# Performance work log

Hardware: AMD Instinct MI355X
Metric: run time of the kernel (lower is better)

## Reference

```python
import jax, jax.numpy as jnp
import numpy as np

N_NODES = 50000
N_EDGES = 800000
F_IN = 128
HID = 128
N_GRAPHS = 256


def setup_inputs() -> dict:
    key = jax.random.key(0)
    ks = jax.random.split(key, 12)
    gx = jax.random.normal(ks[0], (N_NODES, F_IN), dtype=jnp.float32)
    edge_index = jax.random.randint(ks[1], (2, N_EDGES), 0, N_NODES, dtype=jnp.int64)
    batch = jnp.sort(jax.random.randint(ks[2], (N_NODES,), 0, N_GRAPHS, dtype=jnp.int64))
    edge_attr = jax.random.uniform(ks[3], (N_EDGES,), dtype=jnp.float32)
    s1 = 1.0 / np.sqrt(F_IN)
    s2 = 1.0 / np.sqrt(HID)
    W1 = jax.random.uniform(ks[4], (F_IN, HID), jnp.float32, -s1, s1)
    b1 = jnp.zeros((HID,), jnp.float32)
    W2 = jax.random.uniform(ks[5], (HID, HID), jnp.float32, -s2, s2)
    b2 = jnp.zeros((HID,), jnp.float32)
    W3 = jax.random.uniform(ks[6], (HID, HID), jnp.float32, -s2, s2)
    b3 = jnp.zeros((HID,), jnp.float32)
    return {"gx": gx, "edge_index": edge_index, "batch": batch, "edge_attr": edge_attr,
            "W1": W1, "b1": b1, "W2": W2, "b2": b2, "W3": W3, "b3": b3}


def _gcn_conv(x, W, b, row, col, edge_weight, n_nodes):
    # PyG GCNConv with add_self_loops=False:
    #   deg[i] = sum of edge_weight over edges with dst == i
    #   norm_e = deg^{-1/2}[row] * w_e * deg^{-1/2}[col]
    #   out[i] = sum_{e: col_e == i} norm_e * (x @ W)[row_e] + b
    deg = jax.ops.segment_sum(edge_weight, col, num_segments=n_nodes)
    dinv = jnp.where(deg > 0, jax.lax.rsqrt(deg), 0.0)
    norm = dinv[row] * edge_weight * dinv[col]  # [E]
    h = x @ W  # [N, H]
    msg = h[row] * norm[:, None]  # [E, H] gather + scale
    out = jax.ops.segment_sum(msg, col, num_segments=n_nodes)  # scatter-add
    return out + b


def reference(gx, edge_index, batch, edge_attr, W1, b1, W2, b2, W3, b3):
    row, col = edge_index[0], edge_index[1]
    n = gx.shape[0]
    # dropout layers are in eval mode (identity) for a deterministic reference
    h = jax.nn.relu(_gcn_conv(gx, W1, b1, row, col, edge_attr, n))
    h = jax.nn.relu(_gcn_conv(h, W2, b2, row, col, edge_attr, n))
    h = _gcn_conv(h, W3, b3, row, col, edge_attr, n)
    readout = jax.ops.segment_sum(h, batch, num_segments=N_GRAPHS)  # global_add_pool
    return h, readout
```

## Files before the change

kernel.cpp:

```cpp
#include <hip/hip_runtime.h>

#define FEAT 128

typedef __attribute__((ext_vector_type(8))) short short8;
typedef __attribute__((ext_vector_type(4))) float f32x4;

__device__ __forceinline__ unsigned int bf16rtn(float f) {
    unsigned int u = __float_as_uint(f);
    return (u + 0x7fffu + ((u >> 16) & 1u)) >> 16;
}
__device__ __forceinline__ float bf16tof(unsigned int h) { return __uint_as_float(h << 16); }
__device__ __forceinline__ float bf16lo(unsigned int v) { return __uint_as_float(v << 16); }
__device__ __forceinline__ float bf16hi(unsigned int v) { return __uint_as_float(v & 0xffff0000u); }

__global__ __launch_bounds__(256) void hist_kernel(const int* __restrict__ col,
                                                   int* __restrict__ ghist,
                                                   int E, int nblk, int nbuck) {
    __shared__ int h[256];
    const int t = threadIdx.x, b = blockIdx.x;
    h[t] = 0;
    __syncthreads();
    const int base = b * 4096;
#pragma unroll
    for (int i = 0; i < 16; ++i) {
        int e = base + i * 256 + t;
        if (e < E) atomicAdd(&h[col[e] >> 8], 1);
    }
    __syncthreads();
    if (t < nbuck) ghist[t * nblk + b] = h[t];
}

__global__ __launch_bounds__(256) void scan_block_kernel(const int* __restrict__ cnt,
                                                         int* __restrict__ out,
                                                         int* __restrict__ bsum, int M) {
    __shared__ int s[256];
    int t = threadIdx.x;
    int i = blockIdx.x * 256 + t;
    int own = (i < M) ? cnt[i] : 0;
    s[t] = own;
    for (int off = 1; off < 256; off <<= 1) {
        __syncthreads();
        int v = (t >= off) ? s[t - off] : 0;
        __syncthreads();
        s[t] += v;
    }
    __syncthreads();
    if (i < M) out[i] = s[t] - own;
    if (t == 255) bsum[blockIdx.x] = s[255];
}

__global__ __launch_bounds__(256) void scan_bsum_kernel(int* __restrict__ bsum, int nb) {
    __shared__ int s[256];
    int t = threadIdx.x;
    int own = (t < nb) ? bsum[t] : 0;
    s[t] = own;
    for (int off = 1; off < 256; off <<= 1) {
        __syncthreads();
        int v = (t >= off) ? s[t - off] : 0;
        __syncthreads();
        s[t] += v;
    }
    __syncthreads();
    if (t < nb) bsum[t] = s[t] - own;
}

__global__ __launch_bounds__(256) void scatter1_kernel(const int* __restrict__ row,
                                                       const int* __restrict__ col,
                                                       const float* __restrict__ ew,
                                                       const int* __restrict__ gsc,
                                                       const int* __restrict__ bsum,
                                                       uint2* __restrict__ bedge,
                                                       int E, int nblk, int nbuck) {
    __shared__ int cur[256];
    const int t = threadIdx.x, b = blockIdx.x;
    if (t < nbuck) {
        int idx = t * nblk + b;
        cur[t] = gsc[idx] + bsum[idx >> 8];
    }
    __syncthreads();
    const int base = b * 4096;
#pragma unroll
    for (int i = 0; i < 16; ++i) {
        int e = base + i * 256 + t;
        if (e < E) {
            int c = col[e];
            int slot = atomicAdd(&cur[c >> 8], 1);
            bedge[slot] = make_uint2(((unsigned)c << 16) | (unsigned)row[e],
                                     __float_as_uint(ew[e]));
        }
    }
}

__global__ __launch_bounds__(256) void bucket_kernel(const uint2* __restrict__ bedge,
                                                     const int* __restrict__ gsc,
                                                     const int* __restrict__ bsum,
                                                     int* __restrict__ rowptr,
                                                     float* __restrict__ dinv,
                                                     uint2* __restrict__ sedge,
                                                     int N, int E, int nblk, int nbuck) {
    __shared__ int lcnt[256];
    __shared__ float lw[256];
    __shared__ int lscan[256];
    __shared__ int lcur[256];
    __shared__ float ldv[256];

    const int d = blockIdx.x, t = threadIdx.x;
    const int i0 = d * nblk;
    const int base = gsc[i0] + bsum[i0 >> 8];
    int end;
    if (d == nbuck - 1) end = E;
    else {
        const int i1 = (d + 1) * nblk;
        end = gsc[i1] + bsum[i1 >> 8];
    }

    lcnt[t] = 0;
    lw[t] = 0.f;
    __syncthreads();
    for (int i = base + t; i < end; i += 256) {
        uint2 p = bedge[i];
        int c = (p.x >> 16) & 255;
        atomicAdd(&lcnt[c], 1);
        atomicAdd(&lw[c], __uint_as_float(p.y));
    }
    __syncthreads();
    int own = lcnt[t];
    lscan[t] = own;
    for (int off = 1; off < 256; off <<= 1) {
        __syncthreads();
        int v = (t >= off) ? lscan[t - off] : 0;
        __syncthreads();
        lscan[t] += v;
    }
    __syncthreads();
    int excl = lscan[t] - own;
    lcur[t] = base + excl;
    float wsum = lw[t];
    float dv = (wsum > 0.f) ? rsqrtf(wsum) : 0.f;
    ldv[t] = dv;
    int node = d * 256 + t;
    if (node < N) {
        rowptr[node] = base + excl;
        dinv[node] = dv;
    }
    if (d == nbuck - 1 && t == 0) rowptr[N] = E;
    __syncthreads();
    for (int i = base + t; i < end; i += 256) {
        uint2 p = bedge[i];
        int c = (p.x >> 16) & 255;
        int slot = atomicAdd(&lcur[c], 1);
        sedge[slot] = make_uint2(p.x & 0xFFFFu,
                                 __float_as_uint(__uint_as_float(p.y) * ldv[c]));
    }
}

__global__ void convw_kernel(const float* __restrict__ W0, const float* __restrict__ W1,
                             const float* __restrict__ W2,
                             unsigned short* __restrict__ Whi, unsigned short* __restrict__ Wlo) {
    int i = blockIdx.x * blockDim.x + threadIdx.x;
    int which = blockIdx.y;
    const float* W = (which == 0) ? W0 : (which == 1) ? W1 : W2;
    int c = i >> 7, k = i & 127;
    float w = W[(size_t)k * FEAT + c];
    unsigned int h = bf16rtn(w);
    size_t off = (size_t)which * 16384 + (size_t)c * FEAT + k;
    Whi[off] = (unsigned short)h;
    Wlo[off] = (unsigned short)bf16rtn(w - bf16tof(h));
}

__global__ __launch_bounds__(256) void gemm_mfma_kernel(
    const float* __restrict__ X,
    const unsigned short* __restrict__ Wthi, const unsigned short* __restrict__ Wtlo,
    const float* __restrict__ dinv,
    unsigned int* __restrict__ hb,
    int N)
{
    __shared__ unsigned short wh[64 * 128];
    __shared__ unsigned short wl[64 * 128];

    const int tid = threadIdx.x;
    const int r0 = blockIdx.x * 64;
    const int cb = blockIdx.y;

#pragma unroll
    for (int it = 0; it < 4; ++it) {
        int idx = it * 256 + tid;
        int c = idx >> 4;
        int k8 = (idx & 15) * 8;
        int sw = k8 ^ ((c & 7) << 3);
        size_t src = (size_t)(cb * 64 + c) * FEAT + k8;
        *(short8*)&wh[c * 128 + sw] = *(const short8*)(Wthi + src);
        *(short8*)&wl[c * 128 + sw] = *(const short8*)(Wtlo + src);
    }
    __syncthreads();

    const int lane = tid & 63;
    const int wv = tid >> 6;
    const int m = lane & 15;
    const int quad = lane >> 4;
    const int arow = wv * 16 + m;
    const int grow = r0 + arow;
    const float* xrow = X + (size_t)grow * FEAT;

    f32x4 acc[4];
#pragma unroll
    for (int ct = 0; ct < 4; ++ct) acc[ct] = (f32x4){0.f, 0.f, 0.f, 0.f};

#pragma unroll
    for (int kt = 0; kt < 4; ++kt) {
        const int k0 = kt * 32 + quad * 8;
        float4 va = make_float4(0.f, 0.f, 0.f, 0.f);
        float4 vb = make_float4(0.f, 0.f, 0.f, 0.f);
        if (grow < N) {
            va = *(const float4*)(xrow + k0);
            vb = *(const float4*)(xrow + k0 + 4);
        }
        unsigned int h0 = bf16rtn(va.x), h1 = bf16rtn(va.y);
        unsigned int h2 = bf16rtn(va.z), h3 = bf16rtn(va.w);
        unsigned int h4 = bf16rtn(vb.x), h5 = bf16rtn(vb.y);
        unsigned int h6 = bf16rtn(vb.z), h7 = bf16rtn(vb.w);
        short8 ah, al;
        ah[0] = (short)h0; ah[1] = (short)h1; ah[2] = (short)h2; ah[3] = (short)h3;
        ah[4] = (short)h4; ah[5] = (short)h5; ah[6] = (short)h6; ah[7] = (short)h7;
        al[0] = (short)bf16rtn(va.x - bf16tof(h0));
        al[1] = (short)bf16rtn(va.y - bf16tof(h1));
        al[2] = (short)bf16rtn(va.z - bf16tof(h2));
        al[3] = (short)bf16rtn(va.w - bf16tof(h3));
        al[4] = (short)bf16rtn(vb.x - bf16tof(h4));
        al[5] = (short)bf16rtn(vb.y - bf16tof(h5));
        al[6] = (short)bf16rtn(vb.z - bf16tof(h6));
        al[7] = (short)bf16rtn(vb.w - bf16tof(h7));
#pragma unroll
        for (int ct = 0; ct < 4; ++ct) {
            int bc = ct * 16 + m;
            int bw = k0 ^ ((bc & 7) << 3);
            short8 bh = *(const short8*)&wh[bc * 128 + bw];
            short8 bl = *(const short8*)&wl[bc * 128 + bw];
            acc[ct] = __builtin_amdgcn_mfma_f32_16x16x32_bf16(ah, bh, acc[ct], 0, 0, 0);
            acc[ct] = __builtin_amdgcn_mfma_f32_16x16x32_bf16(ah, bl, acc[ct], 0, 0, 0);
            acc[ct] = __builtin_amdgcn_mfma_f32_16x16x32_bf16(al, bh, acc[ct], 0, 0, 0);
        }
    }

    const int rbase = wv * 16 + quad * 4;
    const int grb = r0 + rbase;
    float dv0, dv1, dv2, dv3;
    if (grb + 3 < N) {
        float4 d4 = *(const float4*)(dinv + grb);
        dv0 = d4.x; dv1 = d4.y; dv2 = d4.z; dv3 = d4.w;
    } else {
        dv0 = (grb + 0 < N) ? dinv[grb + 0] : 0.f;
        dv1 = (grb + 1 < N) ? dinv[grb + 1] : 0.f;
        dv2 = (grb + 2 < N) ? dinv[grb + 2] : 0.f;
        dv3 = (grb + 3 < N) ? dinv[grb + 3] : 0.f;
    }

    __syncthreads();
    unsigned short* cl = wh;
#pragma unroll
    for (int ct = 0; ct < 4; ++ct) {
        cl[(rbase + 0) * 72 + ct * 16 + m] = (unsigned short)bf16rtn(acc[ct][0] * dv0);
        cl[(rbase + 1) * 72 + ct * 16 + m] = (unsigned short)bf16rtn(acc[ct][1] * dv1);
        cl[(rbase + 2) * 72 + ct * 16 + m] = (unsigned short)bf16rtn(acc[ct][2] * dv2);
        cl[(rbase + 3) * 72 + ct * 16 + m] = (unsigned short)bf16rtn(acc[ct][3] * dv3);
    }
    __syncthreads();
#pragma unroll
    for (int it = 0; it < 2; ++it) {
        int idx = it * 256 + tid;
        int r = idx >> 3;
        int c4 = (idx & 7) * 4;
        int gr = r0 + r;
        if (gr < N) {
            uint4 pv = *(const uint4*)&cl[r * 72 + c4 * 2];
            *(uint4*)(hb + (size_t)gr * 64 + cb * 32 + c4) = pv;
        }
    }
}

template <int RELU>
__global__ __launch_bounds__(256) void agg_kernel(
    const int* __restrict__ rowptr, const uint2* __restrict__ sedge,
    const uint4* __restrict__ hb4,
    const float* __restrict__ bias,
    float* __restrict__ outX, int N)
{
    const int node = blockIdx.x * 16 + (threadIdx.x >> 4);
    if (node >= N) return;
    const int j = threadIdx.x & 15;
    const int s = rowptr[node];
    const int e = rowptr[node + 1];

    float a0 = 0.f, a1 = 0.f, a2 = 0.f, a3 = 0.f;
    float a4 = 0.f, a5 = 0.f, a6 = 0.f, a7 = 0.f;

    for (int gb = s; gb < e; gb += 8) {
        uint2 m0, m1, m2, m3, m4, m5, m6, m7;
        if (gb + 8 <= e) {
            m0 = sedge[gb + 0]; m1 = sedge[gb + 1];
            m2 = sedge[gb + 2]; m3 = sedge[gb + 3];
            m4 = sedge[gb + 4]; m5 = sedge[gb + 5];
            m6 = sedge[gb + 6]; m7 = sedge[gb + 7];
        } else {
            const uint2 z = make_uint2(0u, 0u);
            m0 = (gb + 0 < e) ? sedge[gb + 0] : z;
            m1 = (gb + 1 < e) ? sedge[gb + 1] : z;
            m2 = (gb + 2 < e) ? sedge[gb + 2] : z;
            m3 = (gb + 3 < e) ? sedge[gb + 3] : z;
            m4 = (gb + 4 < e) ? sedge[gb + 4] : z;
            m5 = (gb + 5 < e) ? sedge[gb + 5] : z;
            m6 = (gb + 6 < e) ? sedge[gb + 6] : z;
            m7 = (gb + 7 < e) ? sedge[gb + 7] : z;
        }
        uint4 v0 = hb4[(size_t)m0.x * 16 + j];
        uint4 v1 = hb4[(size_t)m1.x * 16 + j];
        uint4 v2 = hb4[(size_t)m2.x * 16 + j];
        uint4 v3 = hb4[(size_t)m3.x * 16 + j];
        uint4 v4 = hb4[(size_t)m4.x * 16 + j];
        uint4 v5 = hb4[(size_t)m5.x * 16 + j];
        uint4 v6 = hb4[(size_t)m6.x * 16 + j];
        uint4 v7 = hb4[(size_t)m7.x * 16 + j];
        float w0 = __uint_as_float(m0.y), w1 = __uint_as_float(m1.y);
        float w2 = __uint_as_float(m2.y), w3 = __uint_as_float(m3.y);
        float w4 = __uint_as_float(m4.y), w5 = __uint_as_float(m5.y);
        float w6 = __uint_as_float(m6.y), w7 = __uint_as_float(m7.y);
        a0 = fmaf(w0, bf16lo(v0.x), a0); a1 = fmaf(w0, bf16hi(v0.x), a1);
        a2 = fmaf(w0, bf16lo(v0.y), a2); a3 = fmaf(w0, bf16hi(v0.y), a3);
        a4 = fmaf(w0, bf16lo(v0.z), a4); a5 = fmaf(w0, bf16hi(v0.z), a5);
        a6 = fmaf(w0, bf16lo(v0.w), a6); a7 = fmaf(w0, bf16hi(v0.w), a7);
        a0 = fmaf(w1, bf16lo(v1.x), a0); a1 = fmaf(w1, bf16hi(v1.x), a1);
        a2 = fmaf(w1, bf16lo(v1.y), a2); a3 = fmaf(w1, bf16hi(v1.y), a3);
        a4 = fmaf(w1, bf16lo(v1.z), a4); a5 = fmaf(w1, bf16hi(v1.z), a5);
        a6 = fmaf(w1, bf16lo(v1.w), a6); a7 = fmaf(w1, bf16hi(v1.w), a7);
        a0 = fmaf(w2, bf16lo(v2.x), a0); a1 = fmaf(w2, bf16hi(v2.x), a1);
        a2 = fmaf(w2, bf16lo(v2.y), a2); a3 = fmaf(w2, bf16hi(v2.y), a3);
        a4 = fmaf(w2, bf16lo(v2.z), a4); a5 = fmaf(w2, bf16hi(v2.z), a5);
        a6 = fmaf(w2, bf16lo(v2.w), a6); a7 = fmaf(w2, bf16hi(v2.w), a7);
        a0 = fmaf(w3, bf16lo(v3.x), a0); a1 = fmaf(w3, bf16hi(v3.x), a1);
        a2 = fmaf(w3, bf16lo(v3.y), a2); a3 = fmaf(w3, bf16hi(v3.y), a3);
        a4 = fmaf(w3, bf16lo(v3.z), a4); a5 = fmaf(w3, bf16hi(v3.z), a5);
        a6 = fmaf(w3, bf16lo(v3.w), a6); a7 = fmaf(w3, bf16hi(v3.w), a7);
        a0 = fmaf(w4, bf16lo(v4.x), a0); a1 = fmaf(w4, bf16hi(v4.x), a1);
        a2 = fmaf(w4, bf16lo(v4.y), a2); a3 = fmaf(w4, bf16hi(v4.y), a3);
        a4 = fmaf(w4, bf16lo(v4.z), a4); a5 = fmaf(w4, bf16hi(v4.z), a5);
        a6 = fmaf(w4, bf16lo(v4.w), a6); a7 = fmaf(w4, bf16hi(v4.w), a7);
        a0 = fmaf(w5, bf16lo(v5.x), a0); a1 = fmaf(w5, bf16hi(v5.x), a1);
        a2 = fmaf(w5, bf16lo(v5.y), a2); a3 = fmaf(w5, bf16hi(v5.y), a3);
        a4 = fmaf(w5, bf16lo(v5.z), a4); a5 = fmaf(w5, bf16hi(v5.z), a5);
        a6 = fmaf(w5, bf16lo(v5.w), a6); a7 = fmaf(w5, bf16hi(v5.w), a7);
        a0 = fmaf(w6, bf16lo(v6.x), a0); a1 = fmaf(w6, bf16hi(v6.x), a1);
        a2 = fmaf(w6, bf16lo(v6.y), a2); a3 = fmaf(w6, bf16hi(v6.y), a3);
        a4 = fmaf(w6, bf16lo(v6.z), a4); a5 = fmaf(w6, bf16hi(v6.z), a5);
        a6 = fmaf(w6, bf16lo(v6.w), a6); a7 = fmaf(w6, bf16hi(v6.w), a7);
        a0 = fmaf(w7, bf16lo(v7.x), a0); a1 = fmaf(w7, bf16hi(v7.x), a1);
        a2 = fmaf(w7, bf16lo(v7.y), a2); a3 = fmaf(w7, bf16hi(v7.y), a3);
        a4 = fmaf(w7, bf16lo(v7.z), a4); a5 = fmaf(w7, bf16hi(v7.z), a5);
        a6 = fmaf(w7, bf16lo(v7.w), a6); a7 = fmaf(w7, bf16hi(v7.w), a7);
    }

    float4 bv0 = ((const float4*)bias)[j * 2];
    float4 bv1 = ((const float4*)bias)[j * 2 + 1];
    a0 += bv0.x; a1 += bv0.y; a2 += bv0.z; a3 += bv0.w;
    a4 += bv1.x; a5 += bv1.y; a6 += bv1.z; a7 += bv1.w;
    if (RELU) {
        a0 = fmaxf(a0, 0.f); a1 = fmaxf(a1, 0.f);
        a2 = fmaxf(a2, 0.f); a3 = fmaxf(a3, 0.f);
        a4 = fmaxf(a4, 0.f); a5 = fmaxf(a5, 0.f);
        a6 = fmaxf(a6, 0.f); a7 = fmaxf(a7, 0.f);
    }
    *(float4*)(outX + (size_t)node * FEAT + j * 8)     = make_float4(a0, a1, a2, a3);
    *(float4*)(outX + (size_t)node * FEAT + j * 8 + 4) = make_float4(a4, a5, a6, a7);
}

__global__ __launch_bounds__(256) void readout_kernel(const float* __restrict__ h,
                                                      const int* __restrict__ batch,
                                                      float* __restrict__ ro, int N) {
    __shared__ float part[128];
    const int g = blockIdx.x;
    const int j = threadIdx.x & 127;
    const int half = threadIdx.x >> 7;
    int lo = 0, hi = N;
    while (lo < hi) { int mid = (lo + hi) >> 1; if (batch[mid] < g) lo = mid + 1; else hi = mid; }
    int lo2 = lo, hi2 = N;
    while (lo2 < hi2) { int mid = (lo2 + hi2) >> 1; if (batch[mid] < g + 1) lo2 = mid + 1; else hi2 = mid; }

    float s0 = 0.f, s1 = 0.f;
    int n = lo + half;
    for (; n + 2 < lo2; n += 4) {
        s0 += h[(size_t)n * FEAT + j];
        s1 += h[(size_t)(n + 2) * FEAT + j];
    }
    if (n < lo2) s0 += h[(size_t)n * FEAT + j];
    float s = s0 + s1;
    if (half == 1) part[j] = s;
    __syncthreads();
    if (half == 0) ro[(size_t)g * FEAT + j] = s + part[j];
}

static inline size_t align256(size_t x) { return (x + 255) & ~(size_t)255; }

extern "C" void kernel_launch(void* const* d_in, const int* in_sizes, int n_in,
                              void* d_out, int out_size, void* d_ws, size_t ws_size,
                              hipStream_t stream) {
    const float* gx    = (const float*)d_in[0];
    const int*   ei    = (const int*)d_in[1];
    const int*   batch = (const int*)d_in[2];
    const float* ew    = (const float*)d_in[3];
    const float* W1 = (const float*)d_in[4];
    const float* b1 = (const float*)d_in[5];
    const float* W2 = (const float*)d_in[6];
    const float* b2 = (const float*)d_in[7];
    const float* W3 = (const float*)d_in[8];
    const float* b3 = (const float*)d_in[9];

    const int N = in_sizes[0] / FEAT;
    const int E = in_sizes[3];
    const int G = (out_size - N * FEAT) / FEAT;

    const int* row = ei;
    const int* col = ei + E;

    const int nbuck = (N + 255) >> 8;
    const int nblk  = (E + 4095) >> 12;
    const int M     = nbuck * nblk;

    char* ws = (char*)d_ws;
    int*   rowptr = (int*)ws;         ws += align256((size_t)(N + 1) * 4);
    float* dinv   = (float*)ws;       ws += align256((size_t)N * 4);
    int*   ghist  = (int*)ws;         ws += align256((size_t)M * 4);
    int*   gsc    = (int*)ws;         ws += align256((size_t)M * 4);
    int*   bsum   = (int*)ws;         ws += align256(256 * 4);
    uint2* bedge  = (uint2*)ws;       ws += align256((size_t)E * 8);
    uint2* sedge  = (uint2*)ws;       ws += align256((size_t)E * 8);
    unsigned int* hb = (unsigned int*)ws;  ws += align256((size_t)N * 64 * 4);
    float* bufX   = (float*)ws;       ws += align256((size_t)N * FEAT * 4);
    unsigned short* Wh = (unsigned short*)ws; ws += align256((size_t)3 * 16384 * 2);
    unsigned short* Wl = (unsigned short*)ws; ws += align256((size_t)3 * 16384 * 2);

    float* h_out = (float*)d_out;
    float* ro    = h_out + (size_t)N * FEAT;

    hist_kernel<<<nblk, 256, 0, stream>>>(col, ghist, E, nblk, nbuck);
    const int snb = (M + 255) / 256;
    scan_block_kernel<<<snb, 256, 0, stream>>>(ghist, gsc, bsum, M);
    scan_bsum_kernel<<<1, 256, 0, stream>>>(bsum, snb);
    scatter1_kernel<<<nblk, 256, 0, stream>>>(row, col, ew, gsc, bsum, bedge, E, nblk, nbuck);
    bucket_kernel<<<nbuck, 256, 0, stream>>>(bedge, gsc, bsum, rowptr, dinv, sedge, N, E, nblk, nbuck);

    convw_kernel<<<dim3(64, 3), 256, 0, stream>>>(W1, W2, W3, Wh, Wl);

    dim3 ggrid((N + 63) / 64, 2);
    const int ablocks = (N + 15) / 16;
    const uint4* hb4 = (const uint4*)hb;

    gemm_mfma_kernel<<<ggrid, 256, 0, stream>>>(gx, Wh, Wl, dinv, hb, N);
    agg_kernel<1><<<ablocks, 256, 0, stream>>>(rowptr, sedge, hb4, b1, bufX, N);
    gemm_mfma_kernel<<<ggrid, 256, 0, stream>>>(bufX, Wh + 16384, Wl + 16384, dinv, hb, N);
    agg_kernel<1><<<ablocks, 256, 0, stream>>>(rowptr, sedge, hb4, b2, bufX, N);
    gemm_mfma_kernel<<<ggrid, 256, 0, stream>>>(bufX, Wh + 32768, Wl + 32768, dinv, hb, N);
    agg_kernel<0><<<ablocks, 256, 0, stream>>>(rowptr, sedge, hb4, b3, h_out, N);
    readout_kernel<<<G, 256, 0, stream>>>(h_out, batch, ro, N);
}
```

Before: 285.7 us.

## Fuse CSR build and weight conversion into one cooperative kernel with grid syncs

Merges the histogram, two scan passes, bucket scatter, per-bucket sort/degree computation and the weight bf16 split into a single cooperative-launch kernel that separates phases with grid.sync(). The weight conversion runs on extra blocks alongside the histogram phase. This is meant to remove five kernel launches and their inter-kernel gaps. In exchange it adds grid-wide barrier costs and requires all nblk+16 (~212) blocks to be co-resident, which holds on this GPU but would fail on smaller devices.

```diff
diff --git a/kernel.cpp b/kernel.cpp
--- a/kernel.cpp
+++ b/kernel.cpp
@@ -1,4 +1,5 @@
 #include <hip/hip_runtime.h>
+#include <hip/hip_cooperative_groups.h>
 
 #define FEAT 128
 
@@ -13,159 +14,154 @@
 __device__ __forceinline__ float bf16lo(unsigned int v) { return __uint_as_float(v << 16); }
 __device__ __forceinline__ float bf16hi(unsigned int v) { return __uint_as_float(v & 0xffff0000u); }
 
-__global__ __launch_bounds__(256) void hist_kernel(const int* __restrict__ col,
-                                                   int* __restrict__ ghist,
-                                                   int E, int nblk, int nbuck) {
-    __shared__ int h[256];
+__global__ __launch_bounds__(256) void build_kernel(
+    const int* __restrict__ row, const int* __restrict__ col, const float* __restrict__ ew,
+    const float* __restrict__ W0, const float* __restrict__ W1, const float* __restrict__ W2,
+    unsigned short* __restrict__ Whi, unsigned short* __restrict__ Wlo,
+    int* __restrict__ ghist, int* __restrict__ gsc, int* __restrict__ bsum,
+    uint2* __restrict__ bedge, uint2* __restrict__ sedge,
+    int* __restrict__ rowptr, float* __restrict__ dinv,
+    int N, int E, int nblk, int nbuck, int M, int snb)
+{
+    namespace cg = cooperative_groups;
+    cg::grid_group grid = cg::this_grid();
     const int t = threadIdx.x, b = blockIdx.x;
-    h[t] = 0;
-    __syncthreads();
-    const int base = b * 4096;
-#pragma unroll
-    for (int i = 0; i < 16; ++i) {
-        int e = base + i * 256 + t;
-        if (e < E) atomicAdd(&h[col[e] >> 8], 1);
-    }
-    __syncthreads();
-    if (t < nbuck) ghist[t * nblk + b] = h[t];
-}
-
-__global__ __launch_bounds__(256) void scan_block_kernel(const int* __restrict__ cnt,
-                                                         int* __restrict__ out,
-                                                         int* __restrict__ bsum, int M) {
-    __shared__ int s[256];
-    int t = threadIdx.x;
-    int i = blockIdx.x * 256 + t;
-    int own = (i < M) ? cnt[i] : 0;
-    s[t] = own;
-    for (int off = 1; off < 256; off <<= 1) {
-        __syncthreads();
-        int v = (t >= off) ? s[t - off] : 0;
-        __syncthreads();
-        s[t] += v;
-    }
-    __syncthreads();
-    if (i < M) out[i] = s[t] - own;
-    if (t == 255) bsum[blockIdx.x] = s[255];
-}
-
-__global__ __launch_bounds__(256) void scan_bsum_kernel(int* __restrict__ bsum, int nb) {
-    __shared__ int s[256];
-    int t = threadIdx.x;
-    int own = (t < nb) ? bsum[t] : 0;
-    s[t] = own;
-    for (int off = 1; off < 256; off <<= 1) {
-        __syncthreads();
-        int v = (t >= off) ? s[t - off] : 0;
-        __syncthreads();
-        s[t] += v;
-    }
-    __syncthreads();
-    if (t < nb) bsum[t] = s[t] - own;
-}
-
-__global__ __launch_bounds__(256) void scatter1_kernel(const int* __restrict__ row,
-                                                       const int* __restrict__ col,
-                                                       const float* __restrict__ ew,
-                                                       const int* __restrict__ gsc,
-                                                       const int* __restrict__ bsum,
-                                                       uint2* __restrict__ bedge,
-                                                       int E, int nblk, int nbuck) {
-    __shared__ int cur[256];
-    const int t = threadIdx.x, b = blockIdx.x;
-    if (t < nbuck) {
-        int idx = t * nblk + b;
-        cur[t] = gsc[idx] + bsum[idx >> 8];
-    }
-    __syncthreads();
-    const int base = b * 4096;
-#pragma unroll
-    for (int i = 0; i < 16; ++i) {
-        int e = base + i * 256 + t;
-        if (e < E) {
-            int c = col[e];
-            int slot = atomicAdd(&cur[c >> 8], 1);
-            bedge[slot] = make_uint2(((unsigned)c << 16) | (unsigned)row[e],
-                                     __float_as_uint(ew[e]));
-        }
-    }
-}
-
-__global__ __launch_bounds__(256) void bucket_kernel(const uint2* __restrict__ bedge,
-                                                     const int* __restrict__ gsc,
-                                                     const int* __restrict__ bsum,
-                                                     int* __restrict__ rowptr,
-                                                     float* __restrict__ dinv,
-                                                     uint2* __restrict__ sedge,
-                                                     int N, int E, int nblk, int nbuck) {
-    __shared__ int lcnt[256];
-    __shared__ float lw[256];
-    __shared__ int lscan[256];
-    __shared__ int lcur[256];
-    __shared__ float ldv[256];
-
-    const int d = blockIdx.x, t = threadIdx.x;
-    const int i0 = d * nblk;
-    const int base = gsc[i0] + bsum[i0 >> 8];
-    int end;
-    if (d == nbuck - 1) end = E;
-    else {
-        const int i1 = (d + 1) * nblk;
-        end = gsc[i1] + bsum[i1 >> 8];
-    }
-
-    lcnt[t] = 0;
-    lw[t] = 0.f;
-    __syncthreads();
-    for (int i = base + t; i < end; i += 256) {
-        uint2 p = bedge[i];
-        int c = (p.x >> 16) & 255;
-        atomicAdd(&lcnt[c], 1);
-        atomicAdd(&lw[c], __uint_as_float(p.y));
-    }
-    __syncthreads();
-    int own = lcnt[t];
-    lscan[t] = own;
-    for (int off = 1; off < 256; off <<= 1) {
-        __syncthreads();
-        int v = (t >= off) ? lscan[t - off] : 0;
-        __syncthreads();
-        lscan[t] += v;
-    }
-    __syncthreads();
-    int excl = lscan[t] - own;
-    lcur[t] = base + excl;
-    float wsum = lw[t];
-    float dv = (wsum > 0.f) ? rsqrtf(wsum) : 0.f;
-    ldv[t] = dv;
-    int node = d * 256 + t;
-    if (node < N) {
-        rowptr[node] = base + excl;
-        dinv[node] = dv;
-    }
-    if (d == nbuck - 1 && t == 0) rowptr[N] = E;
-    __syncthreads();
-    for (int i = base + t; i < end; i += 256) {
-        uint2 p = bedge[i];
-        int c = (p.x >> 16) & 255;
-        int slot = atomicAdd(&lcur[c], 1);
-        sedge[slot] = make_uint2(p.x & 0xFFFFu,
-                                 __float_as_uint(__uint_as_float(p.y) * ldv[c]));
-    }
-}
-
-__global__ void convw_kernel(const float* __restrict__ W0, const float* __restrict__ W1,
-                             const float* __restrict__ W2,
-                             unsigned short* __restrict__ Whi, unsigned short* __restrict__ Wlo) {
-    int i = blockIdx.x * blockDim.x + threadIdx.x;
-    int which = blockIdx.y;
-    const float* W = (which == 0) ? W0 : (which == 1) ? W1 : W2;
-    int c = i >> 7, k = i & 127;
-    float w = W[(size_t)k * FEAT + c];
-    unsigned int h = bf16rtn(w);
-    size_t off = (size_t)which * 16384 + (size_t)c * FEAT + k;
-    Whi[off] = (unsigned short)h;
-    Wlo[off] = (unsigned short)bf16rtn(w - bf16tof(h));
+
+    __shared__ int sA[256];
+    __shared__ int sB[256];
+    __shared__ int sC[256];
+    __shared__ float sF[256];
+    __shared__ float sG[256];
+
+    if (b < nblk) {
+        sA[t] = 0;
+        __syncthreads();
+        const int base = b * 4096;
+#pragma unroll
+        for (int i = 0; i < 16; ++i) {
+            int e = base + i * 256 + t;
+            if (e < E) atomicAdd(&sA[col[e] >> 8], 1);
+        }
+        __syncthreads();
+        if (t < nbuck) ghist[t * nblk + b] = sA[t];
+    } else {
+        int bb = b - nblk;
+        if (bb < 16) {
+#pragma unroll
+            for (int q = 0; q < 12; ++q) {
+                int gi = (bb * 12 + q) * 256 + t;
+                int which = gi >> 14;
+                int i = gi & 16383;
+                int c = i >> 7, k = i & 127;
+                const float* W = (which == 0) ? W0 : (which == 1) ? W1 : W2;
+                float w = W[(size_t)k * FEAT + c];
+                unsigned int hh = bf16rtn(w);
+                size_t off = (size_t)which * 16384 + (size_t)c * FEAT + k;
+                Whi[off] = (unsigned short)hh;
+                Wlo[off] = (unsigned short)bf16rtn(w - bf16tof(hh));
+            }
+        }
+    }
+    grid.sync();
+
+    if (b < snb) {
+        int i = b * 256 + t;
+        int own = (i < M) ? ghist[i] : 0;
+        sA[t] = own;
+        for (int off = 1; off < 256; off <<= 1) {
+            __syncthreads();
+            int v = (t >= off) ? sA[t - off] : 0;
+            __syncthreads();
+            sA[t] += v;
+        }
+        __syncthreads();
+        if (i < M) gsc[i] = sA[t] - own;
+        if (t == 255) bsum[b] = sA[255];
+    }
+    grid.sync();
+
+    if (b == 0) {
+        int own = (t < snb) ? bsum[t] : 0;
+        sA[t] = own;
+        for (int off = 1; off < 256; off <<= 1) {
+            __syncthreads();
+            int v = (t >= off) ? sA[t - off] : 0;
+            __syncthreads();
+            sA[t] += v;
+        }
+        __syncthreads();
+        if (t < snb) bsum[t] = sA[t] - own;
+    }
+    grid.sync();
+
+    if (b < nblk) {
+        if (t < nbuck) {
+            int idx = t * nblk + b;
+            sA[t] = gsc[idx] + bsum[idx >> 8];
+        }
+        __syncthreads();
+        const int base = b * 4096;
+#pragma unroll
+        for (int i = 0; i < 16; ++i) {
+            int e = base + i * 256 + t;
+            if (e < E) {
+                int c = col[e];
+                int slot = atomicAdd(&sA[c >> 8], 1);
+                bedge[slot] = make_uint2(((unsigned)c << 16) | (unsigned)row[e],
+                                         __float_as_uint(ew[e]));
+            }
+        }
+    }
+    grid.sync();
+
+    if (b < nbuck) {
+        const int i0 = b * nblk;
+        const int base = gsc[i0] + bsum[i0 >> 8];
+        int end;
+        if (b == nbuck - 1) end = E;
+        else {
+            const int i1 = (b + 1) * nblk;
+            end = gsc[i1] + bsum[i1 >> 8];
+        }
+        sA[t] = 0;
+        sF[t] = 0.f;
+        __syncthreads();
+        for (int i = base + t; i < end; i += 256) {
+            uint2 p = bedge[i];
+            int c = (p.x >> 16) & 255;
+            atomicAdd(&sA[c], 1);
+            atomicAdd(&sF[c], __uint_as_float(p.y));
+        }
+        __syncthreads();
+        int own = sA[t];
+        sB[t] = own;
+        for (int off = 1; off < 256; off <<= 1) {
+            __syncthreads();
+            int v = (t >= off) ? sB[t - off] : 0;
+            __syncthreads();
+            sB[t] += v;
+        }
+        __syncthreads();
+        int excl = sB[t] - own;
+        sC[t] = base + excl;
+        float wsum = sF[t];
+        float dv = (wsum > 0.f) ? rsqrtf(wsum) : 0.f;
+        sG[t] = dv;
+        int node = b * 256 + t;
+        if (node < N) {
+            rowptr[node] = base + excl;
+            dinv[node] = dv;
+        }
+        if (b == nbuck - 1 && t == 0) rowptr[N] = E;
+        __syncthreads();
+        for (int i = base + t; i < end; i += 256) {
+            uint2 p = bedge[i];
+            int c = (p.x >> 16) & 255;
+            int slot = atomicAdd(&sC[c], 1);
+            sedge[slot] = make_uint2(p.x & 0xFFFFu,
+                                     __float_as_uint(__uint_as_float(p.y) * sG[c]));
+        }
+    }
 }
 
 __global__ __launch_bounds__(256) void gemm_mfma_kernel(
@@ -413,16 +409,17 @@
     const float* W3 = (const float*)d_in[8];
     const float* b3 = (const float*)d_in[9];
 
-    const int N = in_sizes[0] / FEAT;
-    const int E = in_sizes[3];
+    int N = in_sizes[0] / FEAT;
+    int E = in_sizes[3];
     const int G = (out_size - N * FEAT) / FEAT;
 
     const int* row = ei;
     const int* col = ei + E;
 
-    const int nbuck = (N + 255) >> 8;
-    const int nblk  = (E + 4095) >> 12;
-    const int M     = nbuck * nblk;
+    int nbuck = (N + 255) >> 8;
+    int nblk  = (E + 4095) >> 12;
+    int M     = nbuck * nblk;
+    int snb   = (M + 255) / 256;
 
     char* ws = (char*)d_ws;
     int*   rowptr = (int*)ws;         ws += align256((size_t)(N + 1) * 4);
@@ -440,14 +437,19 @@
     float* h_out = (float*)d_out;
     float* ro    = h_out + (size_t)N * FEAT;
 
-    hist_kernel<<<nblk, 256, 0, stream>>>(col, ghist, E, nblk, nbuck);
-    const int snb = (M + 255) / 256;
-    scan_block_kernel<<<snb, 256, 0, stream>>>(ghist, gsc, bsum, M);
-    scan_bsum_kernel<<<1, 256, 0, stream>>>(bsum, snb);
-    scatter1_kernel<<<nblk, 256, 0, stream>>>(row, col, ew, gsc, bsum, bedge, E, nblk, nbuck);
-    bucket_kernel<<<nbuck, 256, 0, stream>>>(bedge, gsc, bsum, rowptr, dinv, sedge, N, E, nblk, nbuck);
-
-    convw_kernel<<<dim3(64, 3), 256, 0, stream>>>(W1, W2, W3, Wh, Wl);
+    {
+        void* bargs[] = {
+            (void*)&row, (void*)&col, (void*)&ew,
+            (void*)&W1, (void*)&W2, (void*)&W3,
+            (void*)&Wh, (void*)&Wl,
+            (void*)&ghist, (void*)&gsc, (void*)&bsum,
+            (void*)&bedge, (void*)&sedge, (void*)&rowptr, (void*)&dinv,
+            (void*)&N, (void*)&E, (void*)&nblk, (void*)&nbuck, (void*)&M, (void*)&snb
+        };
+        int gblocks = nblk + 16;
+        hipLaunchCooperativeKernel((void*)build_kernel, dim3(gblocks), dim3(256),
+                                   bargs, 0, stream);
+    }
 
     dim3 ggrid((N + 63) / 64, 2);
     const int ablocks = (N + 15) / 16;
```

Result: slower. 406.2 us (+42.2%).

## Shrink edge-sort chunks, widen bucket blocks, fold weight conversion into histogram

Applied to the files above, without the earlier changes.

Each histogram and scatter block now handles 1024 edges instead of 4096, giving four times as many blocks, and the block-sum scan is extended so one thread covers four entries. The bucket kernel now runs 1024 threads per block, and the scatter stores are 64-bit nontemporal. The weight bf16 split conversion moves into extra blocks of the histogram kernel, which removes one launch. The aim is more parallelism in the preprocessing sort, at the cost of a larger histogram matrix and more scan work.

```diff
diff --git a/kernel.cpp b/kernel.cpp
--- a/kernel.cpp
+++ b/kernel.cpp
@@ -1,6 +1,7 @@
 #include <hip/hip_runtime.h>
 
 #define FEAT 128
+#define EPB 1024
 
 typedef __attribute__((ext_vector_type(8))) short short8;
 typedef __attribute__((ext_vector_type(4))) float f32x4;
@@ -15,14 +16,36 @@
 
 __global__ __launch_bounds__(256) void hist_kernel(const int* __restrict__ col,
                                                    int* __restrict__ ghist,
+                                                   const float* __restrict__ W0,
+                                                   const float* __restrict__ W1,
+                                                   const float* __restrict__ W2,
+                                                   unsigned short* __restrict__ Whi,
+                                                   unsigned short* __restrict__ Wlo,
                                                    int E, int nblk, int nbuck) {
     __shared__ int h[256];
     const int t = threadIdx.x, b = blockIdx.x;
+    if (b >= nblk) {
+        int bb = b - nblk;
+#pragma unroll
+        for (int q = 0; q < 12; ++q) {
+            int gi = (bb * 12 + q) * 256 + t;
+            int which = gi >> 14;
+            int i = gi & 16383;
+            int c = i >> 7, k = i & 127;
+            const float* W = (which == 0) ? W0 : (which == 1) ? W1 : W2;
+            float w = W[(size_t)k * FEAT + c];
+            unsigned int hh = bf16rtn(w);
+            size_t off = (size_t)which * 16384 + (size_t)c * FEAT + k;
+            Whi[off] = (unsigned short)hh;
+            Wlo[off] = (unsigned short)bf16rtn(w - bf16tof(hh));
+        }
+        return;
+    }
     h[t] = 0;
     __syncthreads();
-    const int base = b * 4096;
-#pragma unroll
-    for (int i = 0; i < 16; ++i) {
+    const int base = b * EPB;
+#pragma unroll
+    for (int i = 0; i < 4; ++i) {
         int e = base + i * 256 + t;
         if (e < E) atomicAdd(&h[col[e] >> 8], 1);
     }
@@ -52,8 +75,13 @@
 __global__ __launch_bounds__(256) void scan_bsum_kernel(int* __restrict__ bsum, int nb) {
     __shared__ int s[256];
     int t = threadIdx.x;
-    int own = (t < nb) ? bsum[t] : 0;
-    s[t] = own;
+    int i0 = 4 * t;
+    int v0 = (i0 + 0 < nb) ? bsum[i0 + 0] : 0;
+    int v1 = (i0 + 1 < nb) ? bsum[i0 + 1] : 0;
+    int v2 = (i0 + 2 < nb) ? bsum[i0 + 2] : 0;
+    int v3 = (i0 + 3 < nb) ? bsum[i0 + 3] : 0;
+    int sum = v0 + v1 + v2 + v3;
+    s[t] = sum;
     for (int off = 1; off < 256; off <<= 1) {
         __syncthreads();
         int v = (t >= off) ? s[t - off] : 0;
@@ -61,7 +89,11 @@
         s[t] += v;
     }
     __syncthreads();
-    if (t < nb) bsum[t] = s[t] - own;
+    int excl = s[t] - sum;
+    if (i0 + 0 < nb) bsum[i0 + 0] = excl;
+    if (i0 + 1 < nb) bsum[i0 + 1] = excl + v0;
+    if (i0 + 2 < nb) bsum[i0 + 2] = excl + v0 + v1;
+    if (i0 + 3 < nb) bsum[i0 + 3] = excl + v0 + v1 + v2;
 }
 
 __global__ __launch_bounds__(256) void scatter1_kernel(const int* __restrict__ row,
@@ -78,26 +110,28 @@
         cur[t] = gsc[idx] + bsum[idx >> 8];
     }
     __syncthreads();
-    const int base = b * 4096;
-#pragma unroll
-    for (int i = 0; i < 16; ++i) {
+    const int base = b * EPB;
+#pragma unroll
+    for (int i = 0; i < 4; ++i) {
         int e = base + i * 256 + t;
         if (e < E) {
             int c = col[e];
             int slot = atomicAdd(&cur[c >> 8], 1);
-            bedge[slot] = make_uint2(((unsigned)c << 16) | (unsigned)row[e],
-                                     __float_as_uint(ew[e]));
-        }
-    }
-}
-
-__global__ __launch_bounds__(256) void bucket_kernel(const uint2* __restrict__ bedge,
-                                                     const int* __restrict__ gsc,
-                                                     const int* __restrict__ bsum,
-                                                     int* __restrict__ rowptr,
-                                                     float* __restrict__ dinv,
-                                                     uint2* __restrict__ sedge,
-                                                     int N, int E, int nblk, int nbuck) {
+            unsigned long long pv =
+                ((unsigned long long)__float_as_uint(ew[e]) << 32) |
+                (((unsigned)c << 16) | (unsigned)row[e]);
+            __builtin_nontemporal_store(pv, (unsigned long long*)(bedge + slot));
+        }
+    }
+}
+
+__global__ __launch_bounds__(1024) void bucket_kernel(const uint2* __restrict__ bedge,
+                                                      const int* __restrict__ gsc,
+                                                      const int* __restrict__ bsum,
+                                                      int* __restrict__ rowptr,
+                                                      float* __restrict__ dinv,
+                                                      uint2* __restrict__ sedge,
+                                                      int N, int E, int nblk, int nbuck) {
     __shared__ int lcnt[256];
     __shared__ float lw[256];
     __shared__ int lscan[256];
@@ -114,58 +148,47 @@
         end = gsc[i1] + bsum[i1 >> 8];
     }
 
-    lcnt[t] = 0;
-    lw[t] = 0.f;
-    __syncthreads();
-    for (int i = base + t; i < end; i += 256) {
+    if (t < 256) { lcnt[t] = 0; lw[t] = 0.f; }
+    __syncthreads();
+    for (int i = base + t; i < end; i += 1024) {
         uint2 p = bedge[i];
         int c = (p.x >> 16) & 255;
         atomicAdd(&lcnt[c], 1);
         atomicAdd(&lw[c], __uint_as_float(p.y));
     }
     __syncthreads();
-    int own = lcnt[t];
-    lscan[t] = own;
+    int own = 0;
+    if (t < 256) { own = lcnt[t]; lscan[t] = own; }
     for (int off = 1; off < 256; off <<= 1) {
         __syncthreads();
-        int v = (t >= off) ? lscan[t - off] : 0;
-        __syncthreads();
-        lscan[t] += v;
-    }
-    __syncthreads();
-    int excl = lscan[t] - own;
-    lcur[t] = base + excl;
-    float wsum = lw[t];
-    float dv = (wsum > 0.f) ? rsqrtf(wsum) : 0.f;
-    ldv[t] = dv;
-    int node = d * 256 + t;
-    if (node < N) {
-        rowptr[node] = base + excl;
-        dinv[node] = dv;
-    }
-    if (d == nbuck - 1 && t == 0) rowptr[N] = E;
-    __syncthreads();
-    for (int i = base + t; i < end; i += 256) {
+        int v = (t >= off && t < 256) ? lscan[t - off] : 0;
+        __syncthreads();
+        if (t < 256) lscan[t] += v;
+    }
+    __syncthreads();
+    if (t < 256) {
+        int excl = lscan[t] - own;
+        lcur[t] = base + excl;
+        float wsum = lw[t];
+        float dv = (wsum > 0.f) ? rsqrtf(wsum) : 0.f;
+        ldv[t] = dv;
+        int node = d * 256 + t;
+        if (node < N) {
+            rowptr[node] = base + excl;
+            dinv[node] = dv;
+        }
+        if (d == nbuck - 1 && t == 0) rowptr[N] = E;
+    }
+    __syncthreads();
+    for (int i = base + t; i < end; i += 1024) {
         uint2 p = bedge[i];
         int c = (p.x >> 16) & 255;
         int slot = atomicAdd(&lcur[c], 1);
-        sedge[slot] = make_uint2(p.x & 0xFFFFu,
-                                 __float_as_uint(__uint_as_float(p.y) * ldv[c]));
-    }
-}
-
-__global__ void convw_kernel(const float* __restrict__ W0, const float* __restrict__ W1,
-                             const float* __restrict__ W2,
-                             unsigned short* __restrict__ Whi, unsigned short* __restrict__ Wlo) {
-    int i = blockIdx.x * blockDim.x + threadIdx.x;
-    int which = blockIdx.y;
-    const float* W = (which == 0) ? W0 : (which == 1) ? W1 : W2;
-    int c = i >> 7, k = i & 127;
-    float w = W[(size_t)k * FEAT + c];
-    unsigned int h = bf16rtn(w);
-    size_t off = (size_t)which * 16384 + (size_t)c * FEAT + k;
-    Whi[off] = (unsigned short)h;
-    Wlo[off] = (unsigned short)bf16rtn(w - bf16tof(h));
+        unsigned long long pv =
+            ((unsigned long long)__float_as_uint(__uint_as_float(p.y) * ldv[c]) << 32) |
+            (p.x & 0xFFFFu);
+        __builtin_nontemporal_store(pv, (unsigned long long*)(sedge + slot));
+    }
 }
 
 __global__ __launch_bounds__(256) void gemm_mfma_kernel(
@@ -421,15 +444,16 @@
     const int* col = ei + E;
 
     const int nbuck = (N + 255) >> 8;
-    const int nblk  = (E + 4095) >> 12;
+    const int nblk  = (E + EPB - 1) / EPB;
     const int M     = nbuck * nblk;
+    const int snb   = (M + 255) / 256;
 
     char* ws = (char*)d_ws;
     int*   rowptr = (int*)ws;         ws += align256((size_t)(N + 1) * 4);
     float* dinv   = (float*)ws;       ws += align256((size_t)N * 4);
     int*   ghist  = (int*)ws;         ws += align256((size_t)M * 4);
     int*   gsc    = (int*)ws;         ws += align256((size_t)M * 4);
-    int*   bsum   = (int*)ws;         ws += align256(256 * 4);
+    int*   bsum   = (int*)ws;         ws += align256(1024 * 4);
     uint2* bedge  = (uint2*)ws;       ws += align256((size_t)E * 8);
     uint2* sedge  = (uint2*)ws;       ws += align256((size_t)E * 8);
     unsigned int* hb = (unsigned int*)ws;  ws += align256((size_t)N * 64 * 4);
@@ -440,14 +464,11 @@
     float* h_out = (float*)d_out;
     float* ro    = h_out + (size_t)N * FEAT;
 
-    hist_kernel<<<nblk, 256, 0, stream>>>(col, ghist, E, nblk, nbuck);
-    const int snb = (M + 255) / 256;
+    hist_kernel<<<nblk + 16, 256, 0, stream>>>(col, ghist, W1, W2, W3, Wh, Wl, E, nblk, nbuck);
     scan_block_kernel<<<snb, 256, 0, stream>>>(ghist, gsc, bsum, M);
     scan_bsum_kernel<<<1, 256, 0, stream>>>(bsum, snb);
     scatter1_kernel<<<nblk, 256, 0, stream>>>(row, col, ew, gsc, bsum, bedge, E, nblk, nbuck);
-    bucket_kernel<<<nbuck, 256, 0, stream>>>(bedge, gsc, bsum, rowptr, dinv, sedge, N, E, nblk, nbuck);
-
-    convw_kernel<<<dim3(64, 3), 256, 0, stream>>>(W1, W2, W3, Wh, Wl);
+    bucket_kernel<<<nbuck, 1024, 0, stream>>>(bedge, gsc, bsum, rowptr, dinv, sedge, N, E, nblk, nbuck);
 
     dim3 ggrid((N + 63) / 64, 2);
     const int ablocks = (N + 15) / 16;
```

Result: slower. 310.4 us (+8.7%).
